# Performance work log

Hardware: AMD Instinct MI355X
Metric: run time of the kernel (lower is better)

The kernel has to match this reference:

```python
import jax, jax.numpy as jnp
import numpy as np

M, D, N = 512, 256, 131072  # memory slots, feature dim, num queries


def setup_inputs() -> dict:
    key = jax.random.key(0)
    k1, k2, k3 = jax.random.split(key, 3)
    keys = jax.random.normal(k1, (M, D), dtype=jnp.float32)
    query = jax.random.normal(k2, (N, D), dtype=jnp.float32)
    value = jax.random.normal(k3, (N, D), dtype=jnp.float32)
    return {"keys": keys, "query": query, "value": value}


def _l2_normalize(x, axis, eps=1e-12):
    # matches torch.nn.functional.normalize: x / max(||x||, eps)
    n = jnp.sqrt(jnp.sum(x * x, axis=axis, keepdims=True))
    return x / jnp.maximum(n, eps)


def reference(keys, query, value):
    # score: [n, m]
    score = jnp.matmul(query, keys.T)
    score_query = jax.nn.softmax(score, axis=0)   # softmax over queries
    score_memory = jax.nn.softmax(score, axis=1)  # softmax over memory slots

    # topk(k=1) over dim 1 -> argmax slot per query
    assign = jnp.argmax(score_memory, axis=1)  # [n] int

    # per-slot column max of score_query: [m]
    col_max = jnp.max(score_query, axis=0)

    # weight for each query: score_query[i, assign[i]] / col_max[assign[i]]
    sq_sel = jnp.take_along_axis(score_query, assign[:, None], axis=1)[:, 0]  # [n]
    weight = sq_sel / col_max[assign]  # [n]

    # scatter-reduce weighted values into their assigned slot: [m, d]
    query_updated_memory = jax.ops.segment_sum(
        weight[:, None] * value, assign, num_segments=keys.shape[0]
    )

    updated_memory = _l2_normalize(query_updated_memory + keys, axis=1)
    return updated_memory
```

## Files before the change

### kernel.cpp

```cpp
#include <hip/hip_runtime.h>
#include <hip/hip_bf16.h>
#include <cstdint>
#include <cstddef>

#define NQ 131072
#define MS 512
#define DD 256
#define USPLIT 16
#define WTHR 1e-7f

typedef _Float16 f16;
typedef _Float16 f16x8 __attribute__((ext_vector_type(8)));
typedef float f32x4 __attribute__((ext_vector_type(4)));

__device__ __forceinline__ unsigned enc_f32(float x) {
  unsigned u = __float_as_uint(x);
  return (u & 0x80000000u) ? ~u : (u | 0x80000000u);
}
__device__ __forceinline__ float dec_f32(unsigned u) {
  unsigned b = (u & 0x80000000u) ? (u & 0x7FFFFFFFu) : ~u;
  return __uint_as_float(b);
}

__device__ __forceinline__ void cvt4(const float4 v, uint2& uhi, uint2& ulo) {
  union U { f16 h[4]; uint2 u; } a, b;
  float x;
  x = v.x; a.h[0] = (f16)x; b.h[0] = (f16)(x - (float)a.h[0]);
  x = v.y; a.h[1] = (f16)x; b.h[1] = (f16)(x - (float)a.h[1]);
  x = v.z; a.h[2] = (f16)x; b.h[2] = (f16)(x - (float)a.h[2]);
  x = v.w; a.h[3] = (f16)x; b.h[3] = (f16)(x - (float)a.h[3]);
  uhi = a.u; ulo = b.u;
}

__global__ __launch_bounds__(256) void ksplit_kernel(
    const float* __restrict__ keys, f16* __restrict__ kfh, f16* __restrict__ kfl)
{
  const int t = blockIdx.x * 256 + threadIdx.x;
  const int S = t >> 6, c4 = t & 63;
  const float4 v = *(const float4*)&keys[(size_t)S * DD + c4 * 4];
  const int sch = S >> 8, slot = S & 255;
  const int kq = c4 >> 3, rg = (c4 >> 1) & 3, hf = c4 & 1;
  uint2 uh, ul;
  cvt4(v, uh, ul);
  const size_t off = ((size_t)((sch * 8 + kq) * 4 + rg)) * 4096 + slot * 16 + hf * 8;
  *(uint2*)((char*)kfh + off) = uh;
  *(uint2*)((char*)kfl + off) = ul;
}

#define R_KH 0
#define R_KL 8320
#define R_QH 16640
#define R_QL 24960
#define RSTR 2080

__global__ __launch_bounds__(512, 6) void score_mfma_kernel(
    const float* __restrict__ query,
    const f16* __restrict__ kfh, const f16* __restrict__ kfl,
    unsigned long long* __restrict__ rowPacked,
    unsigned* __restrict__ colmax_enc)
{
  __shared__ __align__(16) unsigned char LDS[36864];

  const int sc = blockIdx.x;
  const int qb = blockIdx.y;
  const int tid = threadIdx.x;
  const int l = tid & 63, wid = tid >> 6;
  const int wq = wid >> 2, ws = wid & 3;
  const int lg = l >> 4, ll = l & 15;
  const int q0 = qb * 128;

  f32x4 acc[4][2];
#pragma unroll
  for (int i = 0; i < 4; ++i)
#pragma unroll
    for (int j = 0; j < 2; ++j) acc[i][j] = (f32x4){0.f, 0.f, 0.f, 0.f};

  const int krg = tid >> 7, kidx = tid & 127;
  const size_t kbase0 = ((size_t)(((sc >> 1) * 8) * 4 + krg)) * 4096
                        + (sc & 1) * 2048 + kidx * 16;
  const int qr0 = tid >> 3, qc0 = tid & 7;
  const int qr1 = (tid + 512) >> 3;
  const int qw0 = (qc0 >> 1) * RSTR + (qc0 & 1) * 8;

  uint4 kh_v, kl_v;
  float4 t4, t5;
  auto loadT = [&](int kq) {
    const size_t koff = kbase0 + (size_t)kq * 16384;
    kh_v = *(const uint4*)((const char*)kfh + koff);
    kl_v = *(const uint4*)((const char*)kfl + koff);
    const int kofs = kq * 32;
    t4 = *(const float4*)&query[(size_t)(q0 + qr0) * DD + kofs + qc0 * 4];
    t5 = *(const float4*)&query[(size_t)(q0 + qr1) * DD + kofs + qc0 * 4];
  };

  loadT(0);
#pragma unroll
  for (int kq = 0; kq < 8; ++kq) {
    __syncthreads();
    {
      uint2 qh0, ql0, qh1, ql1;
      cvt4(t4, qh0, ql0);
      cvt4(t5, qh1, ql1);
      *(uint4*)&LDS[R_KH + krg * RSTR + kidx * 16] = kh_v;
      *(uint4*)&LDS[R_KL + krg * RSTR + kidx * 16] = kl_v;
      *(uint2*)&LDS[R_QH + qw0 + qr0 * 16] = qh0;
      *(uint2*)&LDS[R_QL + qw0 + qr0 * 16] = ql0;
      *(uint2*)&LDS[R_QH + qw0 + qr1 * 16] = qh1;
      *(uint2*)&LDS[R_QL + qw0 + qr1 * 16] = ql1;
    }
    __syncthreads();

    if (kq < 7) loadT(kq + 1);

    f16x8 bh[2], bl[2];
#pragma unroll
    for (int j = 0; j < 2; ++j) {
      const int s = ws * 32 + j * 16 + ll;
      bh[j] = *(const f16x8*)&LDS[R_KH + lg * RSTR + s * 16];
      bl[j] = *(const f16x8*)&LDS[R_KL + lg * RSTR + s * 16];
    }
#pragma unroll
    for (int i = 0; i < 4; ++i) {
      const int r = wq * 64 + i * 16 + ll;
      const f16x8 ah = *(const f16x8*)&LDS[R_QH + lg * RSTR + r * 16];
      const f16x8 al = *(const f16x8*)&LDS[R_QL + lg * RSTR + r * 16];
#pragma unroll
      for (int j = 0; j < 2; ++j) {
        f32x4 c = acc[i][j];
        c = __builtin_amdgcn_mfma_f32_16x16x32_f16(ah, bl[j], c, 0, 0, 0);
        c = __builtin_amdgcn_mfma_f32_16x16x32_f16(al, bh[j], c, 0, 0, 0);
        c = __builtin_amdgcn_mfma_f32_16x16x32_f16(ah, bh[j], c, 0, 0, 0);
        acc[i][j] = c;
      }
    }
  }

  __syncthreads();
  unsigned long long* redRow = (unsigned long long*)(LDS);
  float* redCol = (float*)(LDS + 34816);

#pragma unroll
  for (int i = 0; i < 4; ++i)
#pragma unroll
    for (int v = 0; v < 4; ++v) {
      float bv = acc[i][0][v];
      int bc = ws * 32 + ll;
      {
        const float x = acc[i][1][v];
        const int c = ws * 32 + 16 + ll;
        if (x > bv) { bv = x; bc = c; }
      }
      const int gidx = sc * 128 + bc;
      unsigned long long p =
          ((unsigned long long)enc_f32(bv) << 32) | (unsigned)(~(unsigned)gidx);
      const unsigned long long q = __shfl_xor(p, 1);
      if (q > p) p = q;
      if ((ll & 1) == 0) {
        const int row = wq * 64 + i * 16 + lg * 4 + v;
        redRow[row * 34 + ws * 8 + (ll >> 1)] = p;
      }
    }

#pragma unroll
  for (int j = 0; j < 2; ++j) {
    float m = acc[0][j][0];
#pragma unroll
    for (int i = 0; i < 4; ++i)
#pragma unroll
      for (int v = 0; v < 4; ++v) m = fmaxf(m, acc[i][j][v]);
    m = fmaxf(m, __shfl_xor(m, 16));
    m = fmaxf(m, __shfl_xor(m, 32));
    if (l < 16) redCol[(ws * 32 + j * 16 + l) * 2 + wq] = m;
  }

  __syncthreads();
  if (tid < 128) {
    unsigned long long p = redRow[tid * 34];
#pragma unroll
    for (int w = 1; w < 32; ++w) {
      const unsigned long long q = redRow[tid * 34 + w];
      if (q > p) p = q;
    }
    atomicMax(&rowPacked[(size_t)qb * 128 + tid], p);
    const float v = fmaxf(redCol[tid * 2], redCol[tid * 2 + 1]);
    atomicMax(&colmax_enc[sc * 128 + tid], enc_f32(v));
  }
}

__global__ void weight2_kernel(const unsigned long long* __restrict__ rowPacked,
                               const unsigned* __restrict__ colmax_enc,
                               float* __restrict__ w, int* __restrict__ assign,
                               int* __restrict__ pos, int* __restrict__ count)
{
  const int i = blockIdx.x * blockDim.x + threadIdx.x;
  if (i >= NQ) return;
  const unsigned long long p = rowPacked[i];
  const int a = (int)(~(unsigned)(p & 0xFFFFFFFFull));
  const float sv = dec_f32((unsigned)(p >> 32));
  const float cm = dec_f32(colmax_enc[a]);
  const float wv = expf(sv - cm);
  w[i] = wv;
  assign[i] = a;
  pos[i] = (wv >= WTHR) ? atomicAdd(&count[a], 1) : -1;
}

#define BQ 128
#define BM 128
#define DC 32
#define PAD 132

__global__ __launch_bounds__(256) void score_kernel(
    const float* __restrict__ query, const float* __restrict__ keys,
    int* __restrict__ assign_out, float* __restrict__ sval_out,
    unsigned* __restrict__ colmax_enc)
{
  __shared__ float Qs[DC][PAD];
  __shared__ float Ks[DC][PAD];
  __shared__ float redV[BQ * 16];
  __shared__ int   redI[BQ * 16];

  const int tid = threadIdx.x;
  const int ty = tid >> 4;
  const int tx = tid & 15;
  const int q0 = blockIdx.x * BQ;

  float bestV = -3.4e38f;
  int   bestI = 0;

  for (int mc = 0; mc < MS / BM; ++mc) {
    float acc[8][8];
#pragma unroll
    for (int i = 0; i < 8; ++i)
#pragma unroll
      for (int j = 0; j < 8; ++j) acc[i][j] = 0.f;

    for (int dc = 0; dc < DD; dc += DC) {
      __syncthreads();
#pragma unroll
      for (int it = 0; it < 4; ++it) {
        const int r = (tid >> 3) + it * 32;
        const int d = (tid & 7) * 4;
        const float4 qv = *reinterpret_cast<const float4*>(
            &query[(size_t)(q0 + r) * DD + dc + d]);
        Qs[d + 0][r] = qv.x; Qs[d + 1][r] = qv.y;
        Qs[d + 2][r] = qv.z; Qs[d + 3][r] = qv.w;
        const float4 kv = *reinterpret_cast<const float4*>(
            &keys[(size_t)(mc * BM + r) * DD + dc + d]);
        Ks[d + 0][r] = kv.x; Ks[d + 1][r] = kv.y;
        Ks[d + 2][r] = kv.z; Ks[d + 3][r] = kv.w;
      }
      __syncthreads();
#pragma unroll
      for (int d = 0; d < DC; ++d) {
        float a[8], b[8];
        *reinterpret_cast<float4*>(&a[0]) = *reinterpret_cast<const float4*>(&Qs[d][ty * 8]);
        *reinterpret_cast<float4*>(&a[4]) = *reinterpret_cast<const float4*>(&Qs[d][ty * 8 + 4]);
        *reinterpret_cast<float4*>(&b[0]) = *reinterpret_cast<const float4*>(&Ks[d][tx * 8]);
        *reinterpret_cast<float4*>(&b[4]) = *reinterpret_cast<const float4*>(&Ks[d][tx * 8 + 4]);
#pragma unroll
        for (int i = 0; i < 8; ++i)
#pragma unroll
          for (int j = 0; j < 8; ++j)
            acc[i][j] = fmaf(a[i], b[j], acc[i][j]);
      }
    }

    __syncthreads();
#pragma unroll
    for (int i = 0; i < 8; ++i) {
      float v = acc[i][0]; int jj = 0;
#pragma unroll
      for (int j = 1; j < 8; ++j)
        if (acc[i][j] > v) { v = acc[i][j]; jj = j; }
      redV[(ty * 8 + i) * 16 + tx] = v;
      redI[(ty * 8 + i) * 16 + tx] = mc * BM + tx * 8 + jj;
    }
    __syncthreads();
    if (tid < BQ) {
#pragma unroll
      for (int t = 0; t < 16; ++t) {
        float v = redV[tid * 16 + t];
        if (v > bestV) { bestV = v; bestI = redI[tid * 16 + t]; }
      }
    }
    __syncthreads();
#pragma unroll
    for (int j = 0; j < 8; ++j) {
      float v = acc[0][j];
#pragma unroll
      for (int i = 1; i < 8; ++i) v = fmaxf(v, acc[i][j]);
      redV[(tx * 8 + j) * 16 + ty] = v;
    }
    __syncthreads();
    if (tid < BM) {
      float v = redV[tid * 16];
#pragma unroll
      for (int t = 1; t < 16; ++t) v = fmaxf(v, redV[tid * 16 + t]);
      atomicMax(&colmax_enc[mc * BM + tid], enc_f32(v));
    }
  }

  if (tid < BQ) {
    assign_out[q0 + tid] = bestI;
    sval_out[q0 + tid]   = bestV;
  }
}

__global__ void weight_kernel(const float* __restrict__ sval,
                              const int* __restrict__ assign,
                              const unsigned* __restrict__ colmax_enc,
                              float* __restrict__ w,
                              int* __restrict__ pos,
                              int* __restrict__ count)
{
  int i = blockIdx.x * blockDim.x + threadIdx.x;
  if (i >= NQ) return;
  int a = assign[i];
  float cm = dec_f32(colmax_enc[a]);
  const float wv = expf(sval[i] - cm);
  w[i] = wv;
  pos[i] = (wv >= WTHR) ? atomicAdd(&count[a], 1) : -1;
}


__global__ void scan_kernel(const int* __restrict__ count, int* __restrict__ offset)
{
  __shared__ int s[MS];
  int t = threadIdx.x;
  int c = count[t];
  s[t] = c;
  __syncthreads();
  for (int off = 1; off < MS; off <<= 1) {
    int v = (t >= off) ? s[t - off] : 0;
    __syncthreads();
    s[t] += v;
    __syncthreads();
  }
  offset[t] = s[t] - c;
}

__global__ void fill_kernel(const int* __restrict__ assign,
                            const int* __restrict__ pos,
                            const int* __restrict__ offset,
                            const float* __restrict__ w,
                            int* __restrict__ list,
                            float* __restrict__ wsorted)
{
  int i = blockIdx.x * blockDim.x + threadIdx.x;
  if (i >= NQ) return;
  const int ps = pos[i];
  if (ps < 0) return;
  int a = assign[i];
  const int p = offset[a] + ps;
  list[p] = i;
  wsorted[p] = w[i];
}

__global__ __launch_bounds__(256) void update1_kernel(
    const float* __restrict__ value, const float* __restrict__ wsorted,
    const int* __restrict__ list, const int* __restrict__ offset,
    const int* __restrict__ count, float* __restrict__ partial)
{
  const int m = blockIdx.x, c = blockIdx.y, d = threadIdx.x;
  const int off = offset[m];
  const int cnt = count[m];
  float acc = 0.f;
  int j = c;
  for (; j + USPLIT < cnt; j += 2 * USPLIT) {
    const int i0 = list[off + j];
    const int i1 = list[off + j + USPLIT];
    const float w0 = wsorted[off + j], w1 = wsorted[off + j + USPLIT];
    const float v0 = value[(size_t)i0 * DD + d];
    const float v1 = value[(size_t)i1 * DD + d];
    acc = fmaf(w0, v0, acc);
    acc = fmaf(w1, v1, acc);
  }
  if (j < cnt) {
    const int i = list[off + j];
    acc = fmaf(wsorted[off + j], value[(size_t)i * DD + d], acc);
  }
  partial[((size_t)m * USPLIT + c) * DD + d] = acc;
}

__global__ __launch_bounds__(256) void update2_kernel(
    const float* __restrict__ partial, const float* __restrict__ keys,
    float* __restrict__ out)
{
  const int m = blockIdx.x, d = threadIdx.x;
  float x = keys[(size_t)m * DD + d];
#pragma unroll
  for (int c = 0; c < USPLIT; ++c)
    x += partial[((size_t)m * USPLIT + c) * DD + d];
  float ss = x * x;
#pragma unroll
  for (int o = 1; o < 64; o <<= 1) ss += __shfl_xor(ss, o);
  __shared__ float wsum[4];
  if ((threadIdx.x & 63) == 0) wsum[threadIdx.x >> 6] = ss;
  __syncthreads();
  float tot = wsum[0] + wsum[1] + wsum[2] + wsum[3];
  float den = fmaxf(sqrtf(tot), 1e-12f);
  out[(size_t)m * DD + d] = x / den;
}


extern "C" void kernel_launch(void* const* d_in, const int* in_sizes, int n_in,
                              void* d_out, int out_size, void* d_ws, size_t ws_size,
                              hipStream_t stream)
{
  const float* keys  = (const float*)d_in[0];
  const float* query = (const float*)d_in[1];
  const float* value = (const float*)d_in[2];
  float* out = (float*)d_out;

  char* ws = (char*)d_ws;
  size_t o = 0;
  auto alloc = [&](size_t bytes) -> void* {
    void* p = ws + o;
    o += (bytes + 255) & ~(size_t)255;
    return p;
  };

  f16* kfh = (f16*)alloc((size_t)MS * DD * 2);
  f16* kfl = (f16*)alloc((size_t)MS * DD * 2);
  unsigned long long* rowPacked = (unsigned long long*)alloc((size_t)NQ * 8);
  unsigned* colmax_enc = (unsigned*)alloc(MS * 4);
  int* count  = (int*)alloc(MS * 4);
  int* offset = (int*)alloc(MS * 4);
  int* assign = (int*)alloc((size_t)NQ * 4);
  float* wgt  = (float*)alloc((size_t)NQ * 4);
  int* pos    = (int*)alloc((size_t)NQ * 4);
  int* list   = (int*)alloc((size_t)NQ * 4);
  float* wsorted = (float*)alloc((size_t)NQ * 4);
  float* partial = (float*)alloc((size_t)MS * USPLIT * DD * 4);
  const size_t mfma_need = o;

  if (ws_size >= mfma_need) {
    hipMemsetAsync(rowPacked, 0, (size_t)NQ * 8, stream);
    hipMemsetAsync(colmax_enc, 0, MS * 4, stream);
    hipMemsetAsync(count, 0, MS * 4, stream);

    ksplit_kernel<<<128, 256, 0, stream>>>(keys, kfh, kfl);
    score_mfma_kernel<<<dim3(4, 1024), 512, 0, stream>>>(query, kfh, kfl,
                                                         rowPacked, colmax_enc);
    weight2_kernel<<<NQ / 256, 256, 0, stream>>>(rowPacked, colmax_enc,
                                                 wgt, assign, pos, count);
    scan_kernel<<<1, MS, 0, stream>>>(count, offset);
    fill_kernel<<<NQ / 256, 256, 0, stream>>>(assign, pos, offset, wgt,
                                              list, wsorted);
    update1_kernel<<<dim3(MS, USPLIT), DD, 0, stream>>>(value, wsorted, list,
                                                        offset, count, partial);
    update2_kernel<<<MS, DD, 0, stream>>>(partial, keys, out);
  } else {
    size_t o2 = 0;
    auto alloc2 = [&](size_t bytes) -> void* {
      void* p = ws + o2;
      o2 += (bytes + 255) & ~(size_t)255;
      return p;
    };
    unsigned* colmax2 = (unsigned*)alloc2(MS * 4);
    int* count2  = (int*)alloc2(MS * 4);
    int* offset2 = (int*)alloc2(MS * 4);
    int* assign2 = (int*)alloc2((size_t)NQ * 4);
    float* sval2 = (float*)alloc2((size_t)NQ * 4);
    float* wgt2  = (float*)alloc2((size_t)NQ * 4);
    int* pos2    = (int*)alloc2((size_t)NQ * 4);
    int* list2   = (int*)alloc2((size_t)NQ * 4);
    float* wsorted2 = (float*)alloc2((size_t)NQ * 4);
    float* partial2 = (float*)alloc2((size_t)MS * USPLIT * DD * 4);

    hipMemsetAsync(colmax2, 0, MS * 4, stream);
    hipMemsetAsync(count2, 0, MS * 4, stream);

    score_kernel<<<NQ / BQ, 256, 0, stream>>>(query, keys, assign2, sval2, colmax2);
    weight_kernel<<<NQ / 256, 256, 0, stream>>>(sval2, assign2, colmax2, wgt2, pos2, count2);
    scan_kernel<<<1, MS, 0, stream>>>(count2, offset2);
    fill_kernel<<<NQ / 256, 256, 0, stream>>>(assign2, pos2, offset2, wgt2,
                                              list2, wsorted2);
    update1_kernel<<<dim3(MS, USPLIT), DD, 0, stream>>>(value, wsorted2, list2,
                                                        offset2, count2, partial2);
    update2_kernel<<<MS, DD, 0, stream>>>(partial2, keys, out);
  }
}
```

Before: 165.3 us.

## Load MFMA operands directly from global memory, bypassing LDS staging

The score kernel no longer stages the key and query tiles through shared memory with two barriers per k-step. Each wave now reads its key fragments and query rows straight from global memory into registers and does the fp16 hi/lo split in place. This removes the LDS writes, LDS reads and __syncthreads, but gives up the sharing of loaded data across waves and the software prefetch, so global and L2 traffic rise and load latency is exposed directly.

```diff
diff --git a/kernel.cpp b/kernel.cpp
--- a/kernel.cpp
+++ b/kernel.cpp
@@ -30,6 +30,17 @@
   x = v.z; a.h[2] = (f16)x; b.h[2] = (f16)(x - (float)a.h[2]);
   x = v.w; a.h[3] = (f16)x; b.h[3] = (f16)(x - (float)a.h[3]);
   uhi = a.u; ulo = b.u;
+}
+
+__device__ __forceinline__ void cvt8(const float4 a, const float4 b,
+                                     f16x8& hi, f16x8& lo) {
+  const float v[8] = {a.x, a.y, a.z, a.w, b.x, b.y, b.z, b.w};
+#pragma unroll
+  for (int e = 0; e < 8; ++e) {
+    const f16 h = (f16)v[e];
+    hi[e] = h;
+    lo[e] = (f16)(v[e] - (float)h);
+  }
 }
 
 __global__ __launch_bounds__(256) void ksplit_kernel(
@@ -47,12 +58,6 @@
   *(uint2*)((char*)kfl + off) = ul;
 }
 
-#define R_KH 0
-#define R_KL 8320
-#define R_QH 16640
-#define R_QL 24960
-#define RSTR 2080
-
 __global__ __launch_bounds__(512, 6) void score_mfma_kernel(
     const float* __restrict__ query,
     const f16* __restrict__ kfh, const f16* __restrict__ kfl,
@@ -75,63 +80,34 @@
 #pragma unroll
     for (int j = 0; j < 2; ++j) acc[i][j] = (f32x4){0.f, 0.f, 0.f, 0.f};
 
-  const int krg = tid >> 7, kidx = tid & 127;
-  const size_t kbase0 = ((size_t)(((sc >> 1) * 8) * 4 + krg)) * 4096
-                        + (sc & 1) * 2048 + kidx * 16;
-  const int qr0 = tid >> 3, qc0 = tid & 7;
-  const int qr1 = (tid + 512) >> 3;
-  const int qw0 = (qc0 >> 1) * RSTR + (qc0 & 1) * 8;
-
-  uint4 kh_v, kl_v;
-  float4 t4, t5;
-  auto loadT = [&](int kq) {
-    const size_t koff = kbase0 + (size_t)kq * 16384;
-    kh_v = *(const uint4*)((const char*)kfh + koff);
-    kl_v = *(const uint4*)((const char*)kfl + koff);
-    const int kofs = kq * 32;
-    t4 = *(const float4*)&query[(size_t)(q0 + qr0) * DD + kofs + qc0 * 4];
-    t5 = *(const float4*)&query[(size_t)(q0 + qr1) * DD + kofs + qc0 * 4];
-  };
-
-  loadT(0);
+  const size_t kfrag = (size_t)(sc >> 1) * 131072 + (size_t)lg * 4096
+                     + ((sc & 1) * 128 + ws * 32 + ll) * 16;
+  const float* qbase = query + (size_t)(q0 + wq * 64 + ll) * DD + lg * 8;
+
 #pragma unroll
   for (int kq = 0; kq < 8; ++kq) {
-    __syncthreads();
-    {
-      uint2 qh0, ql0, qh1, ql1;
-      cvt4(t4, qh0, ql0);
-      cvt4(t5, qh1, ql1);
-      *(uint4*)&LDS[R_KH + krg * RSTR + kidx * 16] = kh_v;
-      *(uint4*)&LDS[R_KL + krg * RSTR + kidx * 16] = kl_v;
-      *(uint2*)&LDS[R_QH + qw0 + qr0 * 16] = qh0;
-      *(uint2*)&LDS[R_QL + qw0 + qr0 * 16] = ql0;
-      *(uint2*)&LDS[R_QH + qw0 + qr1 * 16] = qh1;
-      *(uint2*)&LDS[R_QL + qw0 + qr1 * 16] = ql1;
-    }
-    __syncthreads();
-
-    if (kq < 7) loadT(kq + 1);
-
-    f16x8 bh[2], bl[2];
-#pragma unroll
-    for (int j = 0; j < 2; ++j) {
-      const int s = ws * 32 + j * 16 + ll;
-      bh[j] = *(const f16x8*)&LDS[R_KH + lg * RSTR + s * 16];
-      bl[j] = *(const f16x8*)&LDS[R_KL + lg * RSTR + s * 16];
-    }
+    const char* kh = (const char*)kfh + kfrag + (size_t)kq * 16384;
+    const char* kl = (const char*)kfl + kfrag + (size_t)kq * 16384;
+    const f16x8 bh0 = *(const f16x8*)(kh);
+    const f16x8 bl0 = *(const f16x8*)(kl);
+    const f16x8 bh1 = *(const f16x8*)(kh + 256);
+    const f16x8 bl1 = *(const f16x8*)(kl + 256);
+    const float* qk = qbase + kq * 32;
 #pragma unroll
     for (int i = 0; i < 4; ++i) {
-      const int r = wq * 64 + i * 16 + ll;
-      const f16x8 ah = *(const f16x8*)&LDS[R_QH + lg * RSTR + r * 16];
-      const f16x8 al = *(const f16x8*)&LDS[R_QL + lg * RSTR + r * 16];
-#pragma unroll
-      for (int j = 0; j < 2; ++j) {
-        f32x4 c = acc[i][j];
-        c = __builtin_amdgcn_mfma_f32_16x16x32_f16(ah, bl[j], c, 0, 0, 0);
-        c = __builtin_amdgcn_mfma_f32_16x16x32_f16(al, bh[j], c, 0, 0, 0);
-        c = __builtin_amdgcn_mfma_f32_16x16x32_f16(ah, bh[j], c, 0, 0, 0);
-        acc[i][j] = c;
-      }
+      const float* qp = qk + (size_t)(i * 16) * DD;
+      const float4 a0 = *(const float4*)qp;
+      const float4 a1 = *(const float4*)(qp + 4);
+      f16x8 ah, al;
+      cvt8(a0, a1, ah, al);
+      f32x4 c0 = acc[i][0], c1 = acc[i][1];
+      c0 = __builtin_amdgcn_mfma_f32_16x16x32_f16(ah, bl0, c0, 0, 0, 0);
+      c0 = __builtin_amdgcn_mfma_f32_16x16x32_f16(al, bh0, c0, 0, 0, 0);
+      c0 = __builtin_amdgcn_mfma_f32_16x16x32_f16(ah, bh0, c0, 0, 0, 0);
+      c1 = __builtin_amdgcn_mfma_f32_16x16x32_f16(ah, bl1, c1, 0, 0, 0);
+      c1 = __builtin_amdgcn_mfma_f32_16x16x32_f16(al, bh1, c1, 0, 0, 0);
+      c1 = __builtin_amdgcn_mfma_f32_16x16x32_f16(ah, bh1, c1, 0, 0, 0);
+      acc[i][0] = c0; acc[i][1] = c1;
     }
   }
 
```

Result: slower. 315.7 us (+91.0%).
